# Kernel tuning notes

Measured on AMD Instinct MI355X. Metric: run time of the kernel, lower is better.

## Reference

```python
import jax, jax.numpy as jnp
import numpy as np

B, S, HID, H, MAXK = 4, 1024, 1024, 16, 90
D = HID // H


def _rel_emb(emb, q_len, k_len, k):
    # Shaw-style relative position lookup -> [q_len, k_len, head_dim]
    r = jnp.clip(jnp.arange(k_len)[None, :] - jnp.arange(q_len)[:, None], -k, k) + k
    return emb[r]


def setup_inputs() -> dict:
    key = jax.random.key(0)
    ks = jax.random.split(key, 12)
    g = 0.02
    return {
        "query": jax.random.normal(ks[0], (B, S, HID), jnp.float32),
        "key": jax.random.normal(ks[1], (B, S, HID), jnp.float32),
        "value": jax.random.normal(ks[2], (B, S, HID), jnp.float32),
        "mask": jnp.ones((B, 1, S, S), jnp.int32),
        "abs_pos_energy": jax.random.normal(ks[3], (1, H, S, S), jnp.float32),
        "Wq": jax.random.normal(ks[4], (HID, HID), jnp.float32) * g,
        "bq": jnp.zeros((HID,), jnp.float32),
        "Wk": jax.random.normal(ks[5], (HID, HID), jnp.float32) * g,
        "bk": jnp.zeros((HID,), jnp.float32),
        "Wv": jax.random.normal(ks[6], (HID, HID), jnp.float32) * g,
        "bv": jnp.zeros((HID,), jnp.float32),
        "Wo": jax.random.normal(ks[7], (HID, HID), jnp.float32) * g,
        "bo": jnp.zeros((HID,), jnp.float32),
        "rel_k_emb": jax.random.normal(ks[8], (2 * MAXK + 1, D), jnp.float32) * g,
        "rel_v_emb": jax.random.normal(ks[9], (2 * MAXK + 1, D), jnp.float32) * g,
    }


def reference(query, key, value, mask, abs_pos_energy,
              Wq, bq, Wk, bk, Wv, bv, Wo, bo, rel_k_emb, rel_v_emb):
    b, q_len, hid = query.shape
    k_len = key.shape[1]
    d = rel_k_emb.shape[-1]
    h = hid // d
    kmax = (rel_k_emb.shape[0] - 1) // 2
    scale = np.sqrt(d).astype(np.float32)

    Q = (query @ Wq.T + bq).reshape(b, q_len, h, d)   # [b,q,h,d]
    K = (key @ Wk.T + bk).reshape(b, k_len, h, d)
    V = (value @ Wv.T + bv).reshape(b, k_len, h, d)

    r_K = _rel_emb(rel_k_emb, q_len, k_len, kmax)      # [q,k,d]
    r_energy = jnp.einsum('bqhd,qkd->bhqk', Q, r_K)
    energy = jnp.einsum('bqhd,bkhd->bhqk', Q, K)
    energy = (energy + abs_pos_energy + r_energy) / scale
    energy = jnp.where(mask == 0, -1e10, energy)
    attn = jax.nn.softmax(energy, axis=-1)             # [b,h,q,k] (dropout=eval/no-op)

    r_V = _rel_emb(rel_v_emb, q_len, k_len, kmax)      # [q,k,d]
    r_x = jnp.einsum('bhqk,qkd->bqhd', attn, r_V)
    x = jnp.einsum('bhqk,bkhd->bqhd', attn, V)
    x = (x + r_x).reshape(b, q_len, hid)
    return x @ Wo.T + bo
```

## Files before the change

kernel.cpp:

```cpp
#include <hip/hip_runtime.h>

#define BB   4
#define SS   1024
#define HH   16
#define DD   64
#define HID_ 1024
#define MM   4096
#define RR   181
#define KMAX 90

typedef __attribute__((ext_vector_type(8))) short short8;
typedef __attribute__((ext_vector_type(8))) unsigned short ushort8;
typedef __attribute__((ext_vector_type(4))) float f32x4;

__device__ inline unsigned short f2b(float f) {
    unsigned int u = __float_as_uint(f);
    u = u + 0x7fffu + ((u >> 16) & 1u);
    return (unsigned short)(u >> 16);
}
__device__ inline float b2f(unsigned short h) {
    return __uint_as_float(((unsigned int)h) << 16);
}
__device__ inline short8 pack8(float4 a, float4 b) {
    short8 r;
    r[0] = (short)f2b(a.x); r[1] = (short)f2b(a.y);
    r[2] = (short)f2b(a.z); r[3] = (short)f2b(a.w);
    r[4] = (short)f2b(b.x); r[5] = (short)f2b(b.y);
    r[6] = (short)f2b(b.z); r[7] = (short)f2b(b.w);
    return r;
}
#define MFMA(a, b, c) __builtin_amdgcn_mfma_f32_16x16x32_bf16((a), (b), (c), 0, 0, 0)

template<int AF32>
__global__ __launch_bounds__(256) void gemm_mfma(
    const void* __restrict__ Ap0, const void* __restrict__ Ap1, const void* __restrict__ Ap2,
    const float* __restrict__ W0, const float* __restrict__ W1, const float* __restrict__ W2,
    const float* __restrict__ b0, const float* __restrict__ b1, const float* __restrict__ b2,
    void* __restrict__ Cp0, void* __restrict__ Cp1, void* __restrict__ Cp2,
    int kind)
{
    __shared__ ushort Asl[2][128][40];
    __shared__ ushort Wsl[2][128][40];

    const int z = blockIdx.z;
    const void*  Ap   = z == 0 ? Ap0 : (z == 1 ? Ap1 : Ap2);
    const float* W    = z == 0 ? W0  : (z == 1 ? W1  : W2);
    const float* bias = z == 0 ? b0  : (z == 1 ? b1  : b2);
    void*        Cp   = z == 0 ? Cp0 : (z == 1 ? Cp1 : Cp2);

    const int tid = threadIdx.x;
    const int wv = tid >> 6, lane = tid & 63, g = lane >> 4, ln = lane & 15;
    const int wm = wv >> 1, wn = wv & 1;
    const int m0 = blockIdx.y * 128, n0 = blockIdx.x * 128;
    const int srow = tid >> 1, sk0 = (tid & 1) * 16;

    f32x4 acc[4][4];
    f32x4 zz4 = {0.f, 0.f, 0.f, 0.f};
#pragma unroll
    for (int mi = 0; mi < 4; ++mi)
#pragma unroll
        for (int ni = 0; ni < 4; ++ni) acc[mi][ni] = zz4;

    auto STAGE = [&](int d, int t) {
        const int kb = t * 32;
        if (AF32) {
            const float* a = (const float*)Ap + (size_t)(m0 + srow) * HID_ + kb + sk0;
            *(short8*)&Asl[d][srow][sk0]     = pack8(*(const float4*)(a),     *(const float4*)(a + 4));
            *(short8*)&Asl[d][srow][sk0 + 8] = pack8(*(const float4*)(a + 8), *(const float4*)(a + 12));
        } else {
            const ushort* a = (const ushort*)Ap + (size_t)(m0 + srow) * HID_ + kb + sk0;
            *(ushort8*)&Asl[d][srow][sk0]     = *(const ushort8*)(a);
            *(ushort8*)&Asl[d][srow][sk0 + 8] = *(const ushort8*)(a + 8);
        }
        const float* w = W + (size_t)(n0 + srow) * HID_ + kb + sk0;
        *(short8*)&Wsl[d][srow][sk0]     = pack8(*(const float4*)(w),     *(const float4*)(w + 4));
        *(short8*)&Wsl[d][srow][sk0 + 8] = pack8(*(const float4*)(w + 8), *(const float4*)(w + 12));
    };

    STAGE(0, 0);
    for (int t = 0; t < 32; ++t) {
        __syncthreads();
        if (t + 1 < 32) STAGE((t + 1) & 1, t + 1);
        const int cur = t & 1;
        short8 af[4], wf[4];
#pragma unroll
        for (int mi = 0; mi < 4; ++mi) af[mi] = *(const short8*)&Asl[cur][64 * wm + 16 * mi + ln][8 * g];
#pragma unroll
        for (int ni = 0; ni < 4; ++ni) wf[ni] = *(const short8*)&Wsl[cur][64 * wn + 16 * ni + ln][8 * g];
#pragma unroll
        for (int mi = 0; mi < 4; ++mi)
#pragma unroll
            for (int ni = 0; ni < 4; ++ni)
                acc[mi][ni] = MFMA(af[mi], wf[ni], acc[mi][ni]);
    }

#pragma unroll
    for (int ni = 0; ni < 4; ++ni) {
        const int n_g = n0 + 64 * wn + 16 * ni + ln;
        const float bv = bias[n_g];
#pragma unroll
        for (int mi = 0; mi < 4; ++mi) {
#pragma unroll
            for (int rr = 0; rr < 4; ++rr) {
                const int m_g = m0 + 64 * wm + 16 * mi + 4 * g + rr;
                const float v = acc[mi][ni][rr] + bv;
                if (kind == 1) {
                    ((float*)Cp)[(size_t)m_g * HID_ + n_g] = v;
                } else {
                    const int bb = m_g >> 10, s = m_g & 1023, hh = n_g >> 6, dd = n_g & 63;
                    ushort* C = (ushort*)Cp;
                    if (z == 2) C[(((size_t)bb * HH + hh) * DD + dd) * SS + s] = f2b(v);
                    else        C[(((size_t)bb * HH + hh) * SS + s) * DD + dd] = f2b(v);
                }
            }
        }
    }
}

__global__ __launch_bounds__(256) void attn_mfma(
    const ushort* __restrict__ Qh, const ushort* __restrict__ Kh,
    const ushort* __restrict__ Vh, const int* __restrict__ mask,
    const float* __restrict__ absE, const float* __restrict__ relK,
    const float* __restrict__ relV, ushort* __restrict__ X)
{
    __shared__ ushort Kb[2][32][72];
    __shared__ ushort Vt[2][64][40];
    __shared__ ushort QrV[64][200];
    __shared__ ushort sB[64][200];
    __shared__ ushort Ps[4][16][40];
    __shared__ float  m_lds[64];

    const int tid = threadIdx.x;
    const int w = tid >> 6, lane = tid & 63, g = lane >> 4, ln = lane & 15;
    const int qb = blockIdx.x * 64;
    const int bh = blockIdx.y, b = bh >> 4, h = bh & 15;
    const size_t base = (size_t)bh * SS * DD;

    short8 qf0, qf1;
    {
        const ushort* qp = Qh + base + (size_t)(qb + 16 * w + ln) * DD + 8 * g;
        qf0 = *(const short8*)(qp);
        qf1 = *(const short8*)(qp + 32);
    }

    {
        ushort8 zz = {0, 0, 0, 0, 0, 0, 0, 0};
        for (int i = tid; i < 1600; i += 256) ((ushort8*)&sB[0][0])[i] = zz;
    }

#pragma unroll 1
    for (int nt = 0; nt < 12; ++nt) {
        const int r = 16 * nt + ln;
        short8 bf0, bf1;
        if (r < RR) {
            const float* rp = relK + r * DD + 8 * g;
            bf0 = pack8(*(const float4*)(rp),      *(const float4*)(rp + 4));
            bf1 = pack8(*(const float4*)(rp + 32), *(const float4*)(rp + 36));
        } else {
            short8 zz = {0, 0, 0, 0, 0, 0, 0, 0}; bf0 = zz; bf1 = zz;
        }
        f32x4 c = {0.f, 0.f, 0.f, 0.f};
        c = MFMA(qf0, bf0, c);
        c = MFMA(qf1, bf1, c);
#pragma unroll
        for (int rr = 0; rr < 4; ++rr)
            QrV[16 * w + 4 * g + rr][r] = f2b(c[rr]);
    }
    __syncthreads();

    auto STAGEKV = [&](int d, int t) {
        const int kt = t * 32;
        {
            const int kl = tid >> 3, d0 = (tid & 7) * 8;
            *(ushort8*)&Kb[d][kl][d0] = *(const ushort8*)(Kh + base + (size_t)(kt + kl) * DD + d0);
        }
        {
            const int dv = tid >> 2, k0 = (tid & 3) * 8;
            *(ushort8*)&Vt[d][dv][k0] = *(const ushort8*)(Vh + base + (size_t)dv * SS + kt + k0);
        }
    };

    f32x4 acc[4];
    f32x4 zz4 = {0.f, 0.f, 0.f, 0.f};
#pragma unroll
    for (int nt = 0; nt < 4; ++nt) acc[nt] = zz4;
    float mrow[4], lrow[4], Pl[4], Pr[4];
#pragma unroll
    for (int rr = 0; rr < 4; ++rr) { mrow[rr] = -3.0e38f; lrow[rr] = 0.f; Pl[rr] = 0.f; Pr[rr] = 0.f; }

    const int qrow0 = qb + 16 * w + 4 * g;
    const float* aeBase = absE + ((size_t)h * SS + qrow0) * SS;
    const int*   mkBase = mask + ((size_t)b * SS + qrow0) * SS;

    STAGEKV(0, 0);
    for (int t = 0; t < 32; ++t) {
        __syncthreads();
        if (t + 1 < 32) STAGEKV((t + 1) & 1, t + 1);
        const int cur = t & 1;
        const int kt = t * 32;

        f32x4 s0 = zz4, s1 = zz4;
        {
            short8 k00 = *(const short8*)&Kb[cur][ln][8 * g];
            short8 k01 = *(const short8*)&Kb[cur][ln][8 * g + 32];
            short8 k10 = *(const short8*)&Kb[cur][16 + ln][8 * g];
            short8 k11 = *(const short8*)&Kb[cur][16 + ln][8 * g + 32];
            s0 = MFMA(qf0, k00, s0); s0 = MFMA(qf1, k01, s0);
            s1 = MFMA(qf0, k10, s1); s1 = MFMA(qf1, k11, s1);
        }

        float e0[4], e1[4];
#pragma unroll
        for (int rr = 0; rr < 4; ++rr) {
            const int q = qrow0 + rr;
            const size_t ro = (size_t)rr * SS + kt + ln;
            int r0 = kt + ln - q;      r0 = r0 < -KMAX ? -KMAX : (r0 > KMAX ? KMAX : r0);
            int r1 = kt + 16 + ln - q; r1 = r1 < -KMAX ? -KMAX : (r1 > KMAX ? KMAX : r1);
            float v0 = (s0[rr] + aeBase[ro]      + b2f(QrV[16 * w + 4 * g + rr][r0 + KMAX])) * 0.125f;
            float v1 = (s1[rr] + aeBase[ro + 16] + b2f(QrV[16 * w + 4 * g + rr][r1 + KMAX])) * 0.125f;
            if (mkBase[ro] == 0)      v0 = -1e10f;
            if (mkBase[ro + 16] == 0) v1 = -1e10f;
            e0[rr] = v0; e1[rr] = v1;
        }

#pragma unroll
        for (int rr = 0; rr < 4; ++rr) {
            float tmax = fmaxf(e0[rr], e1[rr]);
            tmax = fmaxf(tmax, __shfl_xor(tmax, 1));
            tmax = fmaxf(tmax, __shfl_xor(tmax, 2));
            tmax = fmaxf(tmax, __shfl_xor(tmax, 4));
            tmax = fmaxf(tmax, __shfl_xor(tmax, 8));
            const float mnew = fmaxf(mrow[rr], tmax);
            const float f = __expf(mrow[rr] - mnew);
            mrow[rr] = mnew;
            const float p0 = __expf(e0[rr] - mnew);
            const float p1 = __expf(e1[rr] - mnew);
            float psum = p0 + p1;
            psum += __shfl_xor(psum, 1);
            psum += __shfl_xor(psum, 2);
            psum += __shfl_xor(psum, 4);
            psum += __shfl_xor(psum, 8);
            lrow[rr] = lrow[rr] * f + psum;
            acc[0][rr] *= f; acc[1][rr] *= f; acc[2][rr] *= f; acc[3][rr] *= f;
            Pl[rr] *= f; Pr[rr] *= f;

            const int q = qrow0 + rr;
            const int d0 = kt + ln - q + KMAX;
            const int d1 = kt + 16 + ln - q + KMAX;
            if (d0 <= 0)        Pl[rr] += p0;
            else if (d0 >= 180) Pr[rr] += p0;
            else                sB[16 * w + 4 * g + rr][d0] = f2b(e0[rr]);
            if (d1 <= 0)        Pl[rr] += p1;
            else if (d1 >= 180) Pr[rr] += p1;
            else                sB[16 * w + 4 * g + rr][d1] = f2b(e1[rr]);
            Ps[w][4 * g + rr][ln]      = f2b(p0);
            Ps[w][4 * g + rr][16 + ln] = f2b(p1);
        }

        {
            short8 pa = *(const short8*)&Ps[w][ln][8 * g];
#pragma unroll
            for (int nt = 0; nt < 4; ++nt) {
                short8 vb = *(const short8*)&Vt[cur][16 * nt + ln][8 * g];
                acc[nt] = MFMA(pa, vb, acc[nt]);
            }
        }
    }

#pragma unroll
    for (int rr = 0; rr < 4; ++rr) {
        float pl = Pl[rr], pr = Pr[rr];
        pl += __shfl_xor(pl, 1); pl += __shfl_xor(pl, 2); pl += __shfl_xor(pl, 4); pl += __shfl_xor(pl, 8);
        pr += __shfl_xor(pr, 1); pr += __shfl_xor(pr, 2); pr += __shfl_xor(pr, 4); pr += __shfl_xor(pr, 8);
        if (ln == 0) {
            m_lds[16 * w + 4 * g + rr] = mrow[rr];
            sB[16 * w + 4 * g + rr][0]   = f2b(pl);
            sB[16 * w + 4 * g + rr][180] = f2b(pr);
        }
    }
    __syncthreads();

    {
        ushort8 zz = {0, 0, 0, 0, 0, 0, 0, 0};
        for (int i = tid; i < 1600; i += 256) ((ushort8*)&QrV[0][0])[i] = zz;
    }
    for (int idx = tid; idx < 12800; idx += 256) {
        const int row = idx / 200;
        const int col = idx - row * 200;
        if (col >= 1 && col <= 179) {
            const int k = qb + row + col - KMAX;
            float p = 0.f;
            if (k >= 0 && k < SS) {
                const float e = b2f(((const ushort*)&sB[0][0])[idx]);
                p = __expf(fminf(e - m_lds[row], 0.f));
            }
            ((ushort*)&sB[0][0])[idx] = f2b(p);
        }
    }
    __syncthreads();
    for (int i = tid; i < RR * 16; i += 256) {
        const int dl = i >> 4, d0 = (i & 15) * 4;
        const float4 v = *(const float4*)&relV[dl * DD + d0];
        QrV[d0][dl]     = f2b(v.x); QrV[d0 + 1][dl] = f2b(v.y);
        QrV[d0 + 2][dl] = f2b(v.z); QrV[d0 + 3][dl] = f2b(v.w);
    }
    __syncthreads();

#pragma unroll 1
    for (int c = 0; c < 6; ++c) {
        short8 a = *(const short8*)&sB[16 * w + ln][8 * g + 32 * c];
#pragma unroll
        for (int nt = 0; nt < 4; ++nt) {
            short8 bb = *(const short8*)&QrV[16 * nt + ln][8 * g + 32 * c];
            acc[nt] = MFMA(a, bb, acc[nt]);
        }
    }

#pragma unroll
    for (int rr = 0; rr < 4; ++rr) {
        const float inv = 1.f / lrow[rr];
        const int q = qrow0 + rr;
#pragma unroll
        for (int nt = 0; nt < 4; ++nt) {
            X[((size_t)b * SS + q) * HID_ + h * DD + 16 * nt + ln] = f2b(acc[nt][rr] * inv);
        }
    }
}

extern "C" void kernel_launch(void* const* d_in, const int* in_sizes, int n_in,
                              void* d_out, int out_size, void* d_ws, size_t ws_size,
                              hipStream_t stream)
{
    const float* query = (const float*)d_in[0];
    const float* key   = (const float*)d_in[1];
    const float* value = (const float*)d_in[2];
    const int*   mask  = (const int*)  d_in[3];
    const float* absE  = (const float*)d_in[4];
    const float* Wq    = (const float*)d_in[5];
    const float* bq    = (const float*)d_in[6];
    const float* Wk    = (const float*)d_in[7];
    const float* bk    = (const float*)d_in[8];
    const float* Wv    = (const float*)d_in[9];
    const float* bv    = (const float*)d_in[10];
    const float* Wo    = (const float*)d_in[11];
    const float* bo    = (const float*)d_in[12];
    const float* relK  = (const float*)d_in[13];
    const float* relV  = (const float*)d_in[14];
    float* out = (float*)d_out;

    ushort* ws = (ushort*)d_ws;
    const size_t SZ = (size_t)MM * HID_;
    ushort* Qh = ws;
    ushort* Kh = ws + SZ;
    ushort* Vh = ws + 2 * SZ;
    ushort* Xb = ws + 3 * SZ;

    dim3 blk(256);
    hipLaunchKernelGGL((gemm_mfma<1>), dim3(8, 32, 3), blk, 0, stream,
                       (const void*)query, (const void*)key, (const void*)value,
                       Wq, Wk, Wv, bq, bk, bv,
                       (void*)Qh, (void*)Kh, (void*)Vh, 0);

    hipLaunchKernelGGL(attn_mfma, dim3(16, 64), blk, 0, stream,
                       Qh, Kh, Vh, mask, absE, relK, relV, Xb);

    hipLaunchKernelGGL((gemm_mfma<0>), dim3(8, 32, 1), blk, 0, stream,
                       (const void*)Xb, (const void*)Xb, (const void*)Xb,
                       Wo, Wo, Wo, bo, bo, bo,
                       (void*)out, (void*)out, (void*)out, 1);
}
```

Before: 477.7 us.

## Rewrite attention to register-prefetch K/V tiles and pre-convert GEMM operands to bf16

```diff
diff --git a/kernel.cpp b/kernel.cpp
--- a/kernel.cpp
+++ b/kernel.cpp
@@ -21,6 +21,9 @@
 __device__ inline float b2f(unsigned short h) {
     return __uint_as_float(((unsigned int)h) << 16);
 }
+__device__ inline unsigned int pk2(float a, float b) {
+    return (unsigned int)f2b(a) | ((unsigned int)f2b(b) << 16);
+}
 __device__ inline short8 pack8(float4 a, float4 b) {
     short8 r;
     r[0] = (short)f2b(a.x); r[1] = (short)f2b(a.y);
@@ -31,22 +34,50 @@
 }
 #define MFMA(a, b, c) __builtin_amdgcn_mfma_f32_16x16x32_bf16((a), (b), (c), 0, 0, 0)
 
-template<int AF32>
+__global__ __launch_bounds__(256) void cvt7(
+    const float* __restrict__ q, const float* __restrict__ k, const float* __restrict__ v,
+    const float* __restrict__ wq, const float* __restrict__ wk,
+    const float* __restrict__ wv, const float* __restrict__ wo,
+    ushort* __restrict__ oq, ushort* __restrict__ ok, ushort* __restrict__ ov,
+    ushort* __restrict__ owq, ushort* __restrict__ owk,
+    ushort* __restrict__ owv, ushort* __restrict__ owo)
+{
+    const int y = blockIdx.y;
+    const float* s; ushort* d; int n;
+    switch (y) {
+        case 0: s = q;  d = oq;  n = MM * HID_;   break;
+        case 1: s = k;  d = ok;  n = MM * HID_;   break;
+        case 2: s = v;  d = ov;  n = MM * HID_;   break;
+        case 3: s = wq; d = owq; n = HID_ * HID_; break;
+        case 4: s = wk; d = owk; n = HID_ * HID_; break;
+        case 5: s = wv; d = owv; n = HID_ * HID_; break;
+        default: s = wo; d = owo; n = HID_ * HID_; break;
+    }
+    const int i = (blockIdx.x * 256 + threadIdx.x) * 8;
+    if (i < n) {
+        float4 a = *(const float4*)&s[i];
+        float4 b = *(const float4*)&s[i + 4];
+        *(short8*)&d[i] = pack8(a, b);
+    }
+}
+
+template<int AF32, int WF32>
 __global__ __launch_bounds__(256) void gemm_mfma(
     const void* __restrict__ Ap0, const void* __restrict__ Ap1, const void* __restrict__ Ap2,
-    const float* __restrict__ W0, const float* __restrict__ W1, const float* __restrict__ W2,
+    const void* __restrict__ W0, const void* __restrict__ W1, const void* __restrict__ W2,
     const float* __restrict__ b0, const float* __restrict__ b1, const float* __restrict__ b2,
     void* __restrict__ Cp0, void* __restrict__ Cp1, void* __restrict__ Cp2,
     int kind)
 {
-    __shared__ ushort Asl[2][128][40];
-    __shared__ ushort Wsl[2][128][40];
+    __shared__ ushort gsm[20480];
+#define ASL(dbf, r, c) gsm[(dbf) * 5120 + (r) * 40 + (c)]
+#define WSL(dbf, r, c) gsm[10240 + (dbf) * 5120 + (r) * 40 + (c)]
 
     const int z = blockIdx.z;
-    const void*  Ap   = z == 0 ? Ap0 : (z == 1 ? Ap1 : Ap2);
-    const float* W    = z == 0 ? W0  : (z == 1 ? W1  : W2);
+    const void* Ap    = z == 0 ? Ap0 : (z == 1 ? Ap1 : Ap2);
+    const void* Wp    = z == 0 ? W0  : (z == 1 ? W1  : W2);
     const float* bias = z == 0 ? b0  : (z == 1 ? b1  : b2);
-    void*        Cp   = z == 0 ? Cp0 : (z == 1 ? Cp1 : Cp2);
+    void* Cp          = z == 0 ? Cp0 : (z == 1 ? Cp1 : Cp2);
 
     const int tid = threadIdx.x;
     const int wv = tid >> 6, lane = tid & 63, g = lane >> 4, ln = lane & 15;
@@ -65,16 +96,22 @@
         const int kb = t * 32;
         if (AF32) {
             const float* a = (const float*)Ap + (size_t)(m0 + srow) * HID_ + kb + sk0;
-            *(short8*)&Asl[d][srow][sk0]     = pack8(*(const float4*)(a),     *(const float4*)(a + 4));
-            *(short8*)&Asl[d][srow][sk0 + 8] = pack8(*(const float4*)(a + 8), *(const float4*)(a + 12));
+            *(short8*)&ASL(d, srow, sk0)     = pack8(*(const float4*)(a),     *(const float4*)(a + 4));
+            *(short8*)&ASL(d, srow, sk0 + 8) = pack8(*(const float4*)(a + 8), *(const float4*)(a + 12));
         } else {
             const ushort* a = (const ushort*)Ap + (size_t)(m0 + srow) * HID_ + kb + sk0;
-            *(ushort8*)&Asl[d][srow][sk0]     = *(const ushort8*)(a);
-            *(ushort8*)&Asl[d][srow][sk0 + 8] = *(const ushort8*)(a + 8);
-        }
-        const float* w = W + (size_t)(n0 + srow) * HID_ + kb + sk0;
-        *(short8*)&Wsl[d][srow][sk0]     = pack8(*(const float4*)(w),     *(const float4*)(w + 4));
-        *(short8*)&Wsl[d][srow][sk0 + 8] = pack8(*(const float4*)(w + 8), *(const float4*)(w + 12));
+            *(ushort8*)&ASL(d, srow, sk0)     = *(const ushort8*)(a);
+            *(ushort8*)&ASL(d, srow, sk0 + 8) = *(const ushort8*)(a + 8);
+        }
+        if (WF32) {
+            const float* w = (const float*)Wp + (size_t)(n0 + srow) * HID_ + kb + sk0;
+            *(short8*)&WSL(d, srow, sk0)     = pack8(*(const float4*)(w),     *(const float4*)(w + 4));
+            *(short8*)&WSL(d, srow, sk0 + 8) = pack8(*(const float4*)(w + 8), *(const float4*)(w + 12));
+        } else {
+            const ushort* w = (const ushort*)Wp + (size_t)(n0 + srow) * HID_ + kb + sk0;
+            *(ushort8*)&WSL(d, srow, sk0)     = *(const ushort8*)(w);
+            *(ushort8*)&WSL(d, srow, sk0 + 8) = *(const ushort8*)(w + 8);
+        }
     };
 
     STAGE(0, 0);
@@ -84,9 +121,9 @@
         const int cur = t & 1;
         short8 af[4], wf[4];
 #pragma unroll
-        for (int mi = 0; mi < 4; ++mi) af[mi] = *(const short8*)&Asl[cur][64 * wm + 16 * mi + ln][8 * g];
-#pragma unroll
-        for (int ni = 0; ni < 4; ++ni) wf[ni] = *(const short8*)&Wsl[cur][64 * wn + 16 * ni + ln][8 * g];
+        for (int mi = 0; mi < 4; ++mi) af[mi] = *(const short8*)&ASL(cur, 64 * wm + 16 * mi + ln, 8 * g);
+#pragma unroll
+        for (int ni = 0; ni < 4; ++ni) wf[ni] = *(const short8*)&WSL(cur, 64 * wn + 16 * ni + ln, 8 * g);
 #pragma unroll
         for (int mi = 0; mi < 4; ++mi)
 #pragma unroll
@@ -94,58 +131,101 @@
                 acc[mi][ni] = MFMA(af[mi], wf[ni], acc[mi][ni]);
     }
 
-#pragma unroll
-    for (int ni = 0; ni < 4; ++ni) {
-        const int n_g = n0 + 64 * wn + 16 * ni + ln;
-        const float bv = bias[n_g];
-#pragma unroll
-        for (int mi = 0; mi < 4; ++mi) {
-#pragma unroll
-            for (int rr = 0; rr < 4; ++rr) {
-                const int m_g = m0 + 64 * wm + 16 * mi + 4 * g + rr;
-                const float v = acc[mi][ni][rr] + bv;
-                if (kind == 1) {
-                    ((float*)Cp)[(size_t)m_g * HID_ + n_g] = v;
-                } else {
-                    const int bb = m_g >> 10, s = m_g & 1023, hh = n_g >> 6, dd = n_g & 63;
-                    ushort* C = (ushort*)Cp;
-                    if (z == 2) C[(((size_t)bb * HH + hh) * DD + dd) * SS + s] = f2b(v);
-                    else        C[(((size_t)bb * HH + hh) * SS + s) * DD + dd] = f2b(v);
+    if (kind == 1) {
+#pragma unroll
+        for (int ni = 0; ni < 4; ++ni) {
+            const int n_g = n0 + 64 * wn + 16 * ni + ln;
+            const float bv = bias[n_g];
+#pragma unroll
+            for (int mi = 0; mi < 4; ++mi)
+#pragma unroll
+                for (int rr = 0; rr < 4; ++rr) {
+                    const int m_g = m0 + 64 * wm + 16 * mi + 4 * g + rr;
+                    ((float*)Cp)[(size_t)m_g * HID_ + n_g] = acc[mi][ni][rr] + bv;
                 }
-            }
-        }
-    }
-}
-
-__global__ __launch_bounds__(256) void attn_mfma(
+        }
+    } else if (z != 2) {
+#pragma unroll
+        for (int ni = 0; ni < 4; ++ni) {
+            const int n_g = n0 + 64 * wn + 16 * ni + ln;
+            const float bv = bias[n_g];
+            const int hh = n_g >> 6, dd = n_g & 63;
+#pragma unroll
+            for (int mi = 0; mi < 4; ++mi)
+#pragma unroll
+                for (int rr = 0; rr < 4; ++rr) {
+                    const int m_g = m0 + 64 * wm + 16 * mi + 4 * g + rr;
+                    const int bb = m_g >> 10, s = m_g & 1023;
+                    ((ushort*)Cp)[(((size_t)bb * HH + hh) * SS + s) * DD + dd] =
+                        f2b(acc[mi][ni][rr] + bv);
+                }
+        }
+    } else {
+        __syncthreads();
+#pragma unroll
+        for (int ni = 0; ni < 4; ++ni) {
+            const int n_l = 64 * wn + 16 * ni + ln;
+            const float bv = bias[n0 + n_l];
+#pragma unroll
+            for (int mi = 0; mi < 4; ++mi)
+#pragma unroll
+                for (int rr = 0; rr < 4; ++rr) {
+                    const int m_l = 64 * wm + 16 * mi + 4 * g + rr;
+                    gsm[n_l * 136 + m_l] = f2b(acc[mi][ni][rr] + bv);
+                }
+        }
+        __syncthreads();
+        const int r = tid >> 1, hf = tid & 1;
+        const int n_g = n0 + r, hh = n_g >> 6, dd = n_g & 63;
+        const int bb = m0 >> 10, s0g = (m0 & 1023) + 64 * hf;
+        ushort* dst = (ushort*)Cp + (((size_t)bb * HH + hh) * DD + dd) * SS + s0g;
+        const ushort* src = &gsm[r * 136 + 64 * hf];
+#pragma unroll
+        for (int i = 0; i < 8; ++i)
+            *(ushort8*)&dst[8 * i] = *(const ushort8*)&src[8 * i];
+    }
+#undef ASL
+#undef WSL
+}
+
+struct TileRegs {
+    short8 kf00, kf01, kf10, kf11;
+    short8 vf0, vf1, vf2, vf3;
+    float4 ae0, ae1;
+    int4   mk0, mk1;
+};
+
+__global__ __launch_bounds__(256) void attn2(
     const ushort* __restrict__ Qh, const ushort* __restrict__ Kh,
     const ushort* __restrict__ Vh, const int* __restrict__ mask,
     const float* __restrict__ absE, const float* __restrict__ relK,
     const float* __restrict__ relV, ushort* __restrict__ X)
 {
-    __shared__ ushort Kb[2][32][72];
-    __shared__ ushort Vt[2][64][40];
     __shared__ ushort QrV[64][200];
     __shared__ ushort sB[64][200];
-    __shared__ ushort Ps[4][16][40];
-    __shared__ float  m_lds[64];
+    __shared__ unsigned int Ps32[4][16][20];
+    __shared__ float m_lds[64];
 
     const int tid = threadIdx.x;
     const int w = tid >> 6, lane = tid & 63, g = lane >> 4, ln = lane & 15;
     const int qb = blockIdx.x * 64;
     const int bh = blockIdx.y, b = bh >> 4, h = bh & 15;
     const size_t base = (size_t)bh * SS * DD;
+    const int strow = 16 * w + ln;
+    const int q_stat = qb + strow;
+    const int qrow0 = qb + 16 * w + 4 * g;
 
     short8 qf0, qf1;
     {
-        const ushort* qp = Qh + base + (size_t)(qb + 16 * w + ln) * DD + 8 * g;
+        const ushort* qp = Qh + base + (size_t)q_stat * DD + 8 * g;
         qf0 = *(const short8*)(qp);
         qf1 = *(const short8*)(qp + 32);
     }
 
     {
         ushort8 zz = {0, 0, 0, 0, 0, 0, 0, 0};
-        for (int i = tid; i < 1600; i += 256) ((ushort8*)&sB[0][0])[i] = zz;
+        for (int i = lane; i < 400; i += 64)
+            *(ushort8*)&sB[16 * w + i / 25][(i % 25) * 8] = zz;
     }
 
 #pragma unroll 1
@@ -166,164 +246,162 @@
         for (int rr = 0; rr < 4; ++rr)
             QrV[16 * w + 4 * g + rr][r] = f2b(c[rr]);
     }
+
+    const float* aeBase = absE + ((size_t)h * SS + q_stat) * SS;
+    const int*   mkBase = mask + ((size_t)b * SS + q_stat) * SS;
+
+    f32x4 zz4 = {0.f, 0.f, 0.f, 0.f};
+    f32x4 acc0 = zz4, acc1 = zz4, acc2 = zz4, acc3 = zz4;
+    float mst = -3.0e38f, lst = 0.f, Plc = 0.f, Prc = 0.f;
+
+    auto LOAD = [&](TileRegs& R, int t) {
+        const int kt = 32 * t;
+        const ushort* kp = Kh + base + (size_t)(kt + ln) * DD + 8 * g;
+        R.kf00 = *(const short8*)(kp);
+        R.kf01 = *(const short8*)(kp + 32);
+        R.kf10 = *(const short8*)(kp + 16 * DD);
+        R.kf11 = *(const short8*)(kp + 16 * DD + 32);
+        const ushort* vp = Vh + base + (size_t)ln * SS + kt + 8 * g;
+        R.vf0 = *(const short8*)(vp);
+        R.vf1 = *(const short8*)(vp + 16 * SS);
+        R.vf2 = *(const short8*)(vp + 32 * SS);
+        R.vf3 = *(const short8*)(vp + 48 * SS);
+        const float* ap = aeBase + kt + 4 * g;
+        R.ae0 = *(const float4*)(ap);
+        R.ae1 = *(const float4*)(ap + 16);
+        const int* mp = mkBase + kt + 4 * g;
+        R.mk0 = *(const int4*)(mp);
+        R.mk1 = *(const int4*)(mp + 16);
+    };
+
+    auto COMP = [&](const TileRegs& R, int t) {
+        const int kt = 32 * t;
+        f32x4 s0 = zz4, s1 = zz4;
+        s0 = MFMA(R.kf00, qf0, s0); s0 = MFMA(R.kf01, qf1, s0);
+        s1 = MFMA(R.kf10, qf0, s1); s1 = MFMA(R.kf11, qf1, s1);
+
+        const int db0 = kt + 4 * g - q_stat + KMAX;
+        float e0[4], e1[4];
+#pragma unroll
+        for (int rr = 0; rr < 4; ++rr) {
+            int dc0 = db0 + rr;      dc0 = dc0 < 0 ? 0 : (dc0 > 180 ? 180 : dc0);
+            int dc1 = db0 + 16 + rr; dc1 = dc1 < 0 ? 0 : (dc1 > 180 ? 180 : dc1);
+            float v0 = (s0[rr] + (&R.ae0.x)[rr] + b2f(QrV[strow][dc0])) * 0.125f;
+            float v1 = (s1[rr] + (&R.ae1.x)[rr] + b2f(QrV[strow][dc1])) * 0.125f;
+            if ((&R.mk0.x)[rr] == 0) v0 = -1e10f;
+            if ((&R.mk1.x)[rr] == 0) v1 = -1e10f;
+            e0[rr] = v0; e1[rr] = v1;
+        }
+
+        float tmax = fmaxf(fmaxf(fmaxf(e0[0], e0[1]), fmaxf(e0[2], e0[3])),
+                           fmaxf(fmaxf(e1[0], e1[1]), fmaxf(e1[2], e1[3])));
+        tmax = fmaxf(tmax, __shfl_xor(tmax, 16));
+        tmax = fmaxf(tmax, __shfl_xor(tmax, 32));
+        if (__any(tmax > mst + 8.f)) {
+            const float mn = fmaxf(mst, tmax);
+            const float f = __expf(mst - mn);
+            mst = mn; lst *= f; Plc *= f; Prc *= f;
+#pragma unroll
+            for (int rr = 0; rr < 4; ++rr) {
+                const float fa = __shfl(f, 4 * g + rr);
+                acc0[rr] *= fa; acc1[rr] *= fa; acc2[rr] *= fa; acc3[rr] *= fa;
+            }
+        }
+
+        float p0[4], p1[4], ps = 0.f;
+#pragma unroll
+        for (int rr = 0; rr < 4; ++rr) {
+            p0[rr] = __expf(e0[rr] - mst);
+            p1[rr] = __expf(e1[rr] - mst);
+            ps += p0[rr] + p1[rr];
+        }
+        ps += __shfl_xor(ps, 16);
+        ps += __shfl_xor(ps, 32);
+        lst += ps;
+
+#pragma unroll
+        for (int rr = 0; rr < 4; ++rr) {
+            const int dd0 = db0 + rr, dd1 = db0 + 16 + rr;
+            if (dd0 <= 0)        Plc += p0[rr];
+            else if (dd0 >= 180) Prc += p0[rr];
+            else                 sB[strow][dd0] = f2b(e0[rr]);
+            if (dd1 <= 0)        Plc += p1[rr];
+            else if (dd1 >= 180) Prc += p1[rr];
+            else                 sB[strow][dd1] = f2b(e1[rr]);
+        }
+
+        Ps32[w][ln][2 * g]         = pk2(p0[0], p0[1]);
+        Ps32[w][ln][2 * g + 1]     = pk2(p0[2], p0[3]);
+        Ps32[w][ln][8 + 2 * g]     = pk2(p1[0], p1[1]);
+        Ps32[w][ln][8 + 2 * g + 1] = pk2(p1[2], p1[3]);
+
+        short8 pa = *(const short8*)&Ps32[w][ln][4 * g];
+        acc0 = MFMA(pa, R.vf0, acc0);
+        acc1 = MFMA(pa, R.vf1, acc1);
+        acc2 = MFMA(pa, R.vf2, acc2);
+        acc3 = MFMA(pa, R.vf3, acc3);
+    };
+
+    TileRegs RA, RB;
+    LOAD(RA, 0);
+    for (int t = 0; t < 32; t += 2) {
+        LOAD(RB, t + 1);
+        COMP(RA, t);
+        if (t + 2 < 32) LOAD(RA, t + 2);
+        COMP(RB, t + 1);
+    }
+
+    Plc += __shfl_xor(Plc, 16); Plc += __shfl_xor(Plc, 32);
+    Prc += __shfl_xor(Prc, 16); Prc += __shfl_xor(Prc, 32);
+    if (g == 0) {
+        m_lds[strow] = mst;
+        sB[strow][0]   = f2b(Plc);
+        sB[strow][180] = f2b(Prc);
+    }
     __syncthreads();
 
-    auto STAGEKV = [&](int d, int t) {
-        const int kt = t * 32;
-        {
-            const int kl = tid >> 3, d0 = (tid & 7) * 8;
-            *(ushort8*)&Kb[d][kl][d0] = *(const ushort8*)(Kh + base + (size_t)(kt + kl) * DD + d0);
-        }
-        {
-            const int dv = tid >> 2, k0 = (tid & 3) * 8;
-            *(ushort8*)&Vt[d][dv][k0] = *(const ushort8*)(Vh + base + (size_t)dv * SS + kt + k0);
-        }
-    };
-
-    f32x4 acc[4];
-    f32x4 zz4 = {0.f, 0.f, 0.f, 0.f};
-#pragma unroll
-    for (int nt = 0; nt < 4; ++nt) acc[nt] = zz4;
-    float mrow[4], lrow[4], Pl[4], Pr[4];
-#pragma unroll
-    for (int rr = 0; rr < 4; ++rr) { mrow[rr] = -3.0e38f; lrow[rr] = 0.f; Pl[rr] = 0.f; Pr[rr] = 0.f; }
-
-    const int qrow0 = qb + 16 * w + 4 * g;
-    const float* aeBase = absE + ((size_t)h * SS + qrow0) * SS;
-    const int*   mkBase = mask + ((size_t)b * SS + qrow0) * SS;
-
-    STAGEKV(0, 0);
-    for (int t = 0; t < 32; ++t) {
-        __syncthreads();
-        if (t + 1 < 32) STAGEKV((t + 1) & 1, t + 1);
-        const int cur = t & 1;
-        const int kt = t * 32;
-
-        f32x4 s0 = zz4, s1 = zz4;
-        {
-            short8 k00 = *(const short8*)&Kb[cur][ln][8 * g];
-            short8 k01 = *(const short8*)&Kb[cur][ln][8 * g + 32];
-            short8 k10 = *(const short8*)&Kb[cur][16 + ln][8 * g];
-            short8 k11 = *(const short8*)&Kb[cur][16 + ln][8 * g + 32];
-            s0 = MFMA(qf0, k00, s0); s0 = MFMA(qf1, k01, s0);
-            s1 = MFMA(qf0, k10, s1); s1 = MFMA(qf1, k11, s1);
-        }
-
-        float e0[4], e1[4];
-#pragma unroll
-        for (int rr = 0; rr < 4; ++rr) {
-            const int q = qrow0 + rr;
-            const size_t ro = (size_t)rr * SS + kt + ln;
-            int r0 = kt + ln - q;      r0 = r0 < -KMAX ? -KMAX : (r0 > KMAX ? KMAX : r0);
-            int r1 = kt + 16 + ln - q; r1 = r1 < -KMAX ? -KMAX : (r1 > KMAX ? KMAX : r1);
-            float v0 = (s0[rr] + aeBase[ro]      + b2f(QrV[16 * w + 4 * g + rr][r0 + KMAX])) * 0.125f;
-            float v1 = (s1[rr] + aeBase[ro + 16] + b2f(QrV[16 * w + 4 * g + rr][r1 + KMAX])) * 0.125f;
-            if (mkBase[ro] == 0)      v0 = -1e10f;
-            if (mkBase[ro + 16] == 0) v1 = -1e10f;
-            e0[rr] = v0; e1[rr] = v1;
-        }
-
-#pragma unroll
-        for (int rr = 0; rr < 4; ++rr) {
-            float tmax = fmaxf(e0[rr], e1[rr]);
-            tmax = fmaxf(tmax, __shfl_xor(tmax, 1));
-            tmax = fmaxf(tmax, __shfl_xor(tmax, 2));
-            tmax = fmaxf(tmax, __shfl_xor(tmax, 4));
-            tmax = fmaxf(tmax, __shfl_xor(tmax, 8));
-            const float mnew = fmaxf(mrow[rr], tmax);
-            const float f = __expf(mrow[rr] - mnew);
-            mrow[rr] = mnew;
-            const float p0 = __expf(e0[rr] - mnew);
-            const float p1 = __expf(e1[rr] - mnew);
-            float psum = p0 + p1;
-            psum += __shfl_xor(psum, 1);
-            psum += __shfl_xor(psum, 2);
-            psum += __shfl_xor(psum, 4);
-            psum += __shfl_xor(psum, 8);
-            lrow[rr] = lrow[rr] * f + psum;
-            acc[0][rr] *= f; acc[1][rr] *= f; acc[2][rr] *= f; acc[3][rr] *= f;
-            Pl[rr] *= f; Pr[rr] *= f;
-
-            const int q = qrow0 + rr;
-            const int d0 = kt + ln - q + KMAX;
-            const int d1 = kt + 16 + ln - q + KMAX;
-            if (d0 <= 0)        Pl[rr] += p0;
-            else if (d0 >= 180) Pr[rr] += p0;
-            else                sB[16 * w + 4 * g + rr][d0] = f2b(e0[rr]);
-            if (d1 <= 0)        Pl[rr] += p1;
-            else if (d1 >= 180) Pr[rr] += p1;
-            else                sB[16 * w + 4 * g + rr][d1] = f2b(e1[rr]);
-            Ps[w][4 * g + rr][ln]      = f2b(p0);
-            Ps[w][4 * g + rr][16 + ln] = f2b(p1);
-        }
-
-        {
-            short8 pa = *(const short8*)&Ps[w][ln][8 * g];
-#pragma unroll
-            for (int nt = 0; nt < 4; ++nt) {
-                short8 vb = *(const short8*)&Vt[cur][16 * nt + ln][8 * g];
-                acc[nt] = MFMA(pa, vb, acc[nt]);
-            }
-        }
-    }
-
-#pragma unroll
-    for (int rr = 0; rr < 4; ++rr) {
-        float pl = Pl[rr], pr = Pr[rr];
-        pl += __shfl_xor(pl, 1); pl += __shfl_xor(pl, 2); pl += __shfl_xor(pl, 4); pl += __shfl_xor(pl, 8);
-        pr += __shfl_xor(pr, 1); pr += __shfl_xor(pr, 2); pr += __shfl_xor(pr, 4); pr += __shfl_xor(pr, 8);
-        if (ln == 0) {
-            m_lds[16 * w + 4 * g + rr] = mrow[rr];
-            sB[16 * w + 4 * g + rr][0]   = f2b(pl);
-            sB[16 * w + 4 * g + rr][180] = f2b(pr);
-        }
-    }
-    __syncthreads();
-
-    {
-        ushort8 zz = {0, 0, 0, 0, 0, 0, 0, 0};
-        for (int i = tid; i < 1600; i += 256) ((ushort8*)&QrV[0][0])[i] = zz;
-    }
-    for (int idx = tid; idx < 12800; idx += 256) {
-        const int row = idx / 200;
-        const int col = idx - row * 200;
-        if (col >= 1 && col <= 179) {
-            const int k = qb + row + col - KMAX;
-            float p = 0.f;
-            if (k >= 0 && k < SS) {
-                const float e = b2f(((const ushort*)&sB[0][0])[idx]);
-                p = __expf(fminf(e - m_lds[row], 0.f));
-            }
-            ((ushort*)&sB[0][0])[idx] = f2b(p);
-        }
-    }
-    __syncthreads();
+    for (int idx = tid; idx < 64 * 179; idx += 256) {
+        const int row = idx / 179;
+        const int col = 1 + idx - row * 179;
+        const int k = qb + row + col - KMAX;
+        float p = 0.f;
+        if (k >= 0 && k < SS)
+            p = __expf(b2f(sB[row][col]) - m_lds[row]);
+        sB[row][col] = f2b(p);
+    }
     for (int i = tid; i < RR * 16; i += 256) {
         const int dl = i >> 4, d0 = (i & 15) * 4;
         const float4 v = *(const float4*)&relV[dl * DD + d0];
-        QrV[d0][dl]     = f2b(v.x); QrV[d0 + 1][dl] = f2b(v.y);
+        QrV[d0 + 0][dl] = f2b(v.x); QrV[d0 + 1][dl] = f2b(v.y);
         QrV[d0 + 2][dl] = f2b(v.z); QrV[d0 + 3][dl] = f2b(v.w);
     }
+    for (int i = tid; i < 64 * 19; i += 256)
+        QrV[i / 19][181 + i % 19] = 0;
     __syncthreads();
 
 #pragma unroll 1
     for (int c = 0; c < 6; ++c) {
-        short8 a = *(const short8*)&sB[16 * w + ln][8 * g + 32 * c];
-#pragma unroll
-        for (int nt = 0; nt < 4; ++nt) {
-            short8 bb = *(const short8*)&QrV[16 * nt + ln][8 * g + 32 * c];
-            acc[nt] = MFMA(a, bb, acc[nt]);
-        }
+        short8 a = *(const short8*)&sB[strow][8 * g + 32 * c];
+        short8 b0 = *(const short8*)&QrV[ln][8 * g + 32 * c];
+        short8 b1 = *(const short8*)&QrV[16 + ln][8 * g + 32 * c];
+        short8 b2v = *(const short8*)&QrV[32 + ln][8 * g + 32 * c];
+        short8 b3 = *(const short8*)&QrV[48 + ln][8 * g + 32 * c];
+        acc0 = MFMA(a, b0, acc0);
+        acc1 = MFMA(a, b1, acc1);
+        acc2 = MFMA(a, b2v, acc2);
+        acc3 = MFMA(a, b3, acc3);
     }
 
 #pragma unroll
     for (int rr = 0; rr < 4; ++rr) {
-        const float inv = 1.f / lrow[rr];
+        const float li = __shfl(lst, 4 * g + rr);
+        const float inv = 1.f / li;
         const int q = qrow0 + rr;
-#pragma unroll
-        for (int nt = 0; nt < 4; ++nt) {
-            X[((size_t)b * SS + q) * HID_ + h * DD + 16 * nt + ln] = f2b(acc[nt][rr] * inv);
-        }
+        ushort* xp = X + ((size_t)b * SS + q) * HID_ + h * DD + ln;
+        xp[0]  = f2b(acc0[rr] * inv);
+        xp[16] = f2b(acc1[rr] * inv);
+        xp[32] = f2b(acc2[rr] * inv);
+        xp[48] = f2b(acc3[rr] * inv);
     }
 }
 
@@ -349,23 +427,53 @@
     float* out = (float*)d_out;
 
     ushort* ws = (ushort*)d_ws;
-    const size_t SZ = (size_t)MM * HID_;
-    ushort* Qh = ws;
-    ushort* Kh = ws + SZ;
-    ushort* Vh = ws + 2 * SZ;
-    ushort* Xb = ws + 3 * SZ;
-
+    const size_t SZ  = (size_t)MM * HID_;
+    const size_t WSZ = (size_t)HID_ * HID_;
     dim3 blk(256);
-    hipLaunchKernelGGL((gemm_mfma<1>), dim3(8, 32, 3), blk, 0, stream,
-                       (const void*)query, (const void*)key, (const void*)value,
-                       Wq, Wk, Wv, bq, bk, bv,
-                       (void*)Qh, (void*)Kh, (void*)Vh, 0);
-
-    hipLaunchKernelGGL(attn_mfma, dim3(16, 64), blk, 0, stream,
-                       Qh, Kh, Vh, mask, absE, relK, relV, Xb);
-
-    hipLaunchKernelGGL((gemm_mfma<0>), dim3(8, 32, 1), blk, 0, stream,
-                       (const void*)Xb, (const void*)Xb, (const void*)Xb,
-                       Wo, Wo, Wo, bo, bo, bo,
-                       (void*)out, (void*)out, (void*)out, 1);
-}
+
+    if (ws_size >= (size_t)58 * 1024 * 1024) {
+        ushort* qc = ws;
+        ushort* kc = ws + SZ;
+        ushort* vc = ws + 2 * SZ;
+        ushort* W16 = ws + 3 * SZ;
+        ushort* Qh = ws + 3 * SZ + 4 * WSZ;
+        ushort* Kh = Qh + SZ;
+        ushort* Vh = Kh + SZ;
+        ushort* Xb = qc;
+
+        hipLaunchKernelGGL(cvt7, dim3(2048, 7), blk, 0, stream,
+                           query, key, value, Wq, Wk, Wv, Wo,
+                           qc, kc, vc, W16, W16 + WSZ, W16 + 2 * WSZ, W16 + 3 * WSZ);
+
+        hipLaunchKernelGGL((gemm_mfma<0, 0>), dim3(8, 32, 3), blk, 0, stream,
+                           (const void*)qc, (const void*)kc, (const void*)vc,
+                           (const void*)W16, (const void*)(W16 + WSZ), (const void*)(W16 + 2 * WSZ),
+                           bq, bk, bv, (void*)Qh, (void*)Kh, (void*)Vh, 0);
+
+        hipLaunchKernelGGL(attn2, dim3(16, 64), blk, 0, stream,
+                           Qh, Kh, Vh, mask, absE, relK, relV, Xb);
+
+        hipLaunchKernelGGL((gemm_mfma<0, 0>), dim3(8, 32, 1), blk, 0, stream,
+                           (const void*)Xb, (const void*)Xb, (const void*)Xb,
+                           (const void*)(W16 + 3 * WSZ), (const void*)(W16 + 3 * WSZ), (const void*)(W16 + 3 * WSZ),
+                           bo, bo, bo, (void*)out, (void*)out, (void*)out, 1);
+    } else {
+        ushort* Qh = ws;
+        ushort* Kh = ws + SZ;
+        ushort* Vh = ws + 2 * SZ;
+        ushort* Xb = ws + 3 * SZ;
+
+        hipLaunchKernelGGL((gemm_mfma<1, 1>), dim3(8, 32, 3), blk, 0, stream,
+                           (const void*)query, (const void*)key, (const void*)value,
+                           (const void*)Wq, (const void*)Wk, (const void*)Wv,
+                           bq, bk, bv, (void*)Qh, (void*)Kh, (void*)Vh, 0);
+
+        hipLaunchKernelGGL(attn2, dim3(16, 64), blk, 0, stream,
+                           Qh, Kh, Vh, mask, absE, relK, relV, Xb);
+
+        hipLaunchKernelGGL((gemm_mfma<0, 1>), dim3(8, 32, 1), blk, 0, stream,
+                           (const void*)Xb, (const void*)Xb, (const void*)Xb,
+                           (const void*)Wo, (const void*)Wo, (const void*)Wo,
+                           bo, bo, bo, (void*)out, (void*)out, (void*)out, 1);
+    }
+}
```

Measured after the change: 456.2 us. 4.5% less time.
